# Kernel tuning notes

Measured on AMD Instinct MI355X. Metric: run time of the kernel, lower is better.

## Reference

```python
import jax, jax.numpy as jnp
import numpy as np
import math

D = 1024
H = 16
HEAD_D = D // H  # 64
T = 2048
B = 4


def setup_inputs() -> dict:
    key = jax.random.key(0)
    k1, k2, k3 = jax.random.split(key, 3)
    x = jax.random.normal(k1, (B, T, D), dtype=jnp.float32)
    # c_attn: Linear(d, d + 2*head_d, bias=False) -> weight applied as x @ W
    w_attn = jax.random.normal(k2, (D, D + 2 * HEAD_D), dtype=jnp.float32) * (1.0 / math.sqrt(D))
    w_proj = jax.random.normal(k3, (D, D), dtype=jnp.float32) * (1.0 / math.sqrt(D))
    return {"x": x, "w_attn": w_attn, "w_proj": w_proj}


def reference(x, w_attn, w_proj):
    Bv, Tv, _ = x.shape
    qkv = x @ w_attn  # [B,T,D+2*head_d]
    q = qkv[..., :D].reshape(Bv, Tv, H, HEAD_D).transpose(0, 2, 1, 3)  # [B,H,T,hd]
    k = qkv[..., D:D + HEAD_D]        # [B,T,hd] single shared KV head
    v = qkv[..., D + HEAD_D:]         # [B,T,hd]
    scale = 1.0 / math.sqrt(HEAD_D)
    # att: [B,H,T,T], shared K broadcast over H query heads
    att = jnp.einsum('bhqd,bkd->bhqk', q, k) * scale
    causal = jnp.tril(jnp.ones((Tv, Tv), dtype=bool))  # [T,T]
    att = jnp.where(causal[None, None, :, :], att, -jnp.inf)
    att = jax.nn.softmax(att, axis=-1)
    y = jnp.einsum('bhqk,bkd->bhqd', att, v)           # [B,H,T,hd]
    y = y.transpose(0, 2, 1, 3).reshape(Bv, Tv, D)     # [B,T,D]
    return y @ w_proj
```

## Files before the change

kernel.cpp:

```cpp
#include <hip/hip_runtime.h>

typedef unsigned short u16;
typedef unsigned int u32;
typedef __attribute__((ext_vector_type(8))) short short8;
typedef __attribute__((ext_vector_type(4))) float f32x4;
typedef __attribute__((ext_vector_type(4))) u16 u16x4;

__device__ __forceinline__ u16 f2bf(float f) {
  union { float f; unsigned u; } x; x.f = f;
  unsigned r = (x.u + 0x7fffu + ((x.u >> 16) & 1u)) >> 16;
  return (u16)r;
}

__device__ __forceinline__ u16 f2bf_rna(float f) {
  union { float f; u32 u; } x; x.f = f;
  return (u16)((x.u + 0x8000u) >> 16);
}

__device__ __forceinline__ f32x4 mfma16(short8 a, short8 b, f32x4 c) {
  return __builtin_amdgcn_mfma_f32_16x16x32_bf16(a, b, c, 0, 0, 0);
}

__device__ __forceinline__ void gload16(const u16* g, u16* l) {
  __builtin_amdgcn_global_load_lds((const __attribute__((address_space(1))) void*)g,
                                   (__attribute__((address_space(3))) void*)l, 16, 0, 0);
}

__global__ __launch_bounds__(256) void prep(const float* __restrict__ x,
                                            const float* __restrict__ w_attn,
                                            const float* __restrict__ w_proj,
                                            u16* __restrict__ xb,
                                            u16* __restrict__ wat,
                                            u16* __restrict__ wpt) {
  __shared__ float tile[32][33];
  const int bid = blockIdx.x, tid = threadIdx.x;
  if (bid >= 2176) {
    const int id = bid - 2176;
    const f32x4* src = (const f32x4*)(x + (size_t)id * 4096);
    u16x4* dst = (u16x4*)(xb + (size_t)id * 4096);
#pragma unroll
    for (int c = 0; c < 4; ++c) {
      f32x4 v = src[c * 256 + tid];
      u16x4 o;
#pragma unroll
      for (int j = 0; j < 4; ++j) o[j] = f2bf(v[j]);
      dst[c * 256 + tid] = o;
    }
    return;
  }
  const float* src; u16* dst; int C, bx, by;
  if (bid < 1152) { src = w_attn; dst = wat; C = 1152; bx = bid % 36; by = bid / 36; }
  else { int id = bid - 1152; src = w_proj; dst = wpt; C = 1024; bx = id & 31; by = id >> 5; }
  const int R = 1024;
  const int tx = tid & 31, ty = tid >> 5;
  int c = bx * 32 + tx, r0 = by * 32;
#pragma unroll
  for (int i = 0; i < 32; i += 8)
    tile[ty + i][tx] = src[(size_t)(r0 + ty + i) * C + c];
  __syncthreads();
  int oc = r0 + tx, orow0 = bx * 32;
#pragma unroll
  for (int i = 0; i < 32; i += 8)
    dst[(size_t)(orow0 + ty + i) * R + oc] = f2bf(tile[tx][ty + i]);
}

template <bool C_F32, bool VT>
__global__ __launch_bounds__(256) void gemm_bt(const u16* __restrict__ A,
                                               const u16* __restrict__ Bt,
                                               void* __restrict__ Cp,
                                               u16* __restrict__ vt,
                                               int lda, int ldb, int ldc, int K) {
  __shared__ u16 As[2][128 * 32];
  __shared__ u16 Bs[2][128 * 32];
  const int tid = threadIdx.x;
  const int wid = tid >> 6, lane = tid & 63;
  const int quad = lane >> 4, l15 = lane & 15;
  const int m0 = blockIdx.x * 128, n0 = blockIdx.y * 128;
  const int wm = (wid & 1) * 64, wn = (wid >> 1) * 64;
  const int sr = tid >> 2;
  const int sc = (tid & 3) * 8;

  f32x4 acc[4][4] = {};

  auto stage = [&](int t, int bb) {
    const int k0 = t << 5;
#pragma unroll
    for (int cch = 0; cch < 2; ++cch) {
      const int row = sr + cch * 64;
      gload16(A + (size_t)(m0 + row) * lda + k0 + sc, &As[bb][wid * 512 + cch * 2048]);
      gload16(Bt + (size_t)(n0 + row) * ldb + k0 + sc, &Bs[bb][wid * 512 + cch * 2048]);
    }
  };

  const int nk = K >> 5;
  stage(0, 0);
  for (int t = 0; t < nk; ++t) {
    const int bb = t & 1;
    __syncthreads();
    if (t + 1 < nk) stage(t + 1, bb ^ 1);
    short8 a[4], b[4];
#pragma unroll
    for (int i = 0; i < 4; ++i) a[i] = *(const short8*)&As[bb][(wm + 16 * i + l15) * 32 + quad * 8];
#pragma unroll
    for (int j = 0; j < 4; ++j) b[j] = *(const short8*)&Bs[bb][(wn + 16 * j + l15) * 32 + quad * 8];
#pragma unroll
    for (int i = 0; i < 4; ++i)
#pragma unroll
      for (int j = 0; j < 4; ++j)
        acc[i][j] = mfma16(a[i], b[j], acc[i][j]);
  }

#pragma unroll
  for (int i = 0; i < 4; ++i) {
#pragma unroll
    for (int j = 0; j < 4; ++j) {
      const int mrow = m0 + wm + 16 * i + quad * 4;
      const int ncol = n0 + wn + 16 * j + l15;
#pragma unroll
      for (int r = 0; r < 4; ++r) {
        float v = acc[i][j][r];
        if (C_F32) {
          ((float*)Cp)[(size_t)(mrow + r) * ldc + ncol] = v;
        } else {
          u16 hv = f2bf(v);
          ((u16*)Cp)[(size_t)(mrow + r) * ldc + ncol] = hv;
          if (VT) {
            if (ncol >= 1088) {
              int mg = mrow + r;
              int bb2 = mg >> 11, tt = mg & 2047;
              vt[(size_t)(bb2 * 64 + (ncol - 1088)) * 2048 + tt] = hv;
            }
          }
        }
      }
    }
  }
}

__global__ __launch_bounds__(256) void attn_kernel(const u16* __restrict__ qkv,
                                                   const u16* __restrict__ vt,
                                                   u16* __restrict__ y) {
  const int T = 2048, LD = 1152;
  __shared__ u16 Ks[64 * 68];
  __shared__ u16 Vts[64 * 68];
  __shared__ u16 Pw[4][2][16 * 68];

  const int bid = blockIdx.x;
  const int qt = 15 - (bid >> 6);
  const int bh = bid & 63, b = bh >> 4, h = bh & 15;
  const int q0 = qt * 128;
  const int tid = threadIdx.x, wid = tid >> 6, lane = tid & 63;
  const int quad = lane >> 4, l15 = lane & 15;
  const int wq = wid * 32;
  const u16* qkvb = qkv + (size_t)b * T * LD;
  const u16* vtb = vt + (size_t)b * 64 * 2048;
  const int sr0 = tid >> 3, sc0 = (tid & 7) * 8;
  const int sr1 = sr0 + 32;
  const float c1 = 0.18033688f;
  const float M = 18.0f;
  short8 ones;
#pragma unroll
  for (int j = 0; j < 8; ++j) ones[j] = (short)0x3F80;

  short8 qreg[2][2];
#pragma unroll
  for (int jt = 0; jt < 2; ++jt)
#pragma unroll
    for (int ks = 0; ks < 2; ++ks)
      qreg[jt][ks] = *(const short8*)(qkvb + (size_t)(q0 + wq + 16 * jt + l15) * LD + h * 64 + ks * 32 + quad * 8);

  f32x4 acc[4][2] = {};
  f32x4 accs[2] = {};

  short8 kr0 = *(const short8*)(qkvb + (size_t)sr0 * LD + 1024 + sc0);
  short8 kr1 = *(const short8*)(qkvb + (size_t)sr1 * LD + 1024 + sc0);
  short8 vr0 = *(const short8*)(vtb + (size_t)sr0 * 2048 + sc0);
  short8 vr1 = *(const short8*)(vtb + (size_t)sr1 * 2048 + sc0);

  const int ktmax = 2 * qt + 2;
  for (int kt = 0; kt < ktmax; ++kt) {
    const int kv0 = kt * 64;
    __syncthreads();
    *(short8*)&Ks[sr0 * 68 + sc0] = kr0;
    *(short8*)&Ks[sr1 * 68 + sc0] = kr1;
    *(short8*)&Vts[sr0 * 68 + sc0] = vr0;
    *(short8*)&Vts[sr1 * 68 + sc0] = vr1;
    __syncthreads();
    if (kt + 1 < ktmax) {
      const int nv0 = kv0 + 64;
      kr0 = *(const short8*)(qkvb + (size_t)(nv0 + sr0) * LD + 1024 + sc0);
      kr1 = *(const short8*)(qkvb + (size_t)(nv0 + sr1) * LD + 1024 + sc0);
      vr0 = *(const short8*)(vtb + (size_t)sr0 * 2048 + nv0 + sc0);
      vr1 = *(const short8*)(vtb + (size_t)sr1 * 2048 + nv0 + sc0);
    }
    if (kv0 > q0 + wq + 31) continue;

    f32x4 st[4][2] = {};
#pragma unroll
    for (int ks = 0; ks < 2; ++ks) {
      short8 kf[4];
#pragma unroll
      for (int i = 0; i < 4; ++i) kf[i] = *(const short8*)&Ks[(16 * i + l15) * 68 + ks * 32 + quad * 8];
#pragma unroll
      for (int i = 0; i < 4; ++i)
#pragma unroll
        for (int jt = 0; jt < 2; ++jt)
          st[i][jt] = mfma16(kf[i], qreg[jt][ks], st[i][jt]);
    }

    const bool needMask = (kv0 + 63 > q0 + wq);
#pragma unroll
    for (int jt = 0; jt < 2; ++jt) {
      u16* pw = &Pw[wid][jt][0];
      const int qg = q0 + wq + 16 * jt + l15;
#pragma unroll
      for (int i = 0; i < 4; ++i) {
        u16x4 pk;
#pragma unroll
        for (int r = 0; r < 4; ++r) {
          float p = __builtin_amdgcn_exp2f(fmaf(st[i][jt][r], c1, -M));
          if (needMask && (kv0 + 16 * i + quad * 4 + r > qg)) p = 0.f;
          pk[r] = f2bf_rna(p);
        }
        *(u16x4*)&pw[l15 * 68 + 16 * i + quad * 4] = pk;
      }
    }

#pragma unroll
    for (int ks = 0; ks < 2; ++ks) {
      short8 pf[2];
#pragma unroll
      for (int jt = 0; jt < 2; ++jt)
        pf[jt] = *(const short8*)&Pw[wid][jt][l15 * 68 + ks * 32 + quad * 8];
#pragma unroll
      for (int id = 0; id < 4; ++id) {
        short8 vf = *(const short8*)&Vts[(16 * id + l15) * 68 + ks * 32 + quad * 8];
        acc[id][0] = mfma16(vf, pf[0], acc[id][0]);
        acc[id][1] = mfma16(vf, pf[1], acc[id][1]);
      }
      accs[0] = mfma16(ones, pf[0], accs[0]);
      accs[1] = mfma16(ones, pf[1], accs[1]);
    }
  }

#pragma unroll
  for (int jt = 0; jt < 2; ++jt) {
    const float inv = 1.f / accs[jt][0];
    const int qg = q0 + wq + 16 * jt + l15;
#pragma unroll
    for (int id = 0; id < 4; ++id) {
      u16x4 o;
#pragma unroll
      for (int r = 0; r < 4; ++r) o[r] = f2bf(acc[id][jt][r] * inv);
      *(u16x4*)(y + (size_t)(b * T + qg) * 1024 + h * 64 + 16 * id + quad * 4) = o;
    }
  }
}

extern "C" void kernel_launch(void* const* d_in, const int* in_sizes, int n_in,
                              void* d_out, int out_size, void* d_ws, size_t ws_size,
                              hipStream_t stream) {
  const float* x = (const float*)d_in[0];
  const float* w_attn = (const float*)d_in[1];
  const float* w_proj = (const float*)d_in[2];
  float* out = (float*)d_out;
  char* ws = (char*)d_ws;

  u16* wat = (u16*)ws;
  u16* wpt = (u16*)(ws + 2359296);
  u16* xb  = (u16*)(ws + 4456448);
  u16* qkv = (u16*)(ws + 21233664);
  u16* vt  = (u16*)(ws + 40108032);
  u16* y   = (u16*)(ws + 41156608);

  prep<<<dim3(4224), dim3(256), 0, stream>>>(x, w_attn, w_proj, xb, wat, wpt);
  gemm_bt<false, true><<<dim3(64, 9), 256, 0, stream>>>(xb, wat, qkv, vt, 1024, 1024, 1152, 1024);
  attn_kernel<<<dim3(1024), dim3(256), 0, stream>>>(qkv, vt, y);
  gemm_bt<true, false><<<dim3(64, 8), 256, 0, stream>>>(y, wpt, out, nullptr, 1024, 1024, 1024, 1024);
}
```

Baseline: 209.4 us.

## Halve P scratch LDS, use packed bf16 convert, target five blocks per SM

The per-wave P staging buffer shrinks from two 16-row tiles to one, reused sequentially for the two query sub-tiles, which cuts shared memory per block. Float-to-bf16 conversion now uses the hardware v_cvt_pk_bf16_f32 instruction instead of manual integer rounding. Launch bounds request a minimum of five blocks per CU. Together these aim to raise occupancy and trim ALU work in the softmax stage, at the cost of extra LDS round trips and register pressure limits that could cause spills.

```diff
diff --git a/kernel.cpp b/kernel.cpp
--- a/kernel.cpp
+++ b/kernel.cpp
@@ -5,16 +5,12 @@
 typedef __attribute__((ext_vector_type(8))) short short8;
 typedef __attribute__((ext_vector_type(4))) float f32x4;
 typedef __attribute__((ext_vector_type(4))) u16 u16x4;
+typedef __attribute__((ext_vector_type(2))) u32 u32x2;
 
 __device__ __forceinline__ u16 f2bf(float f) {
   union { float f; unsigned u; } x; x.f = f;
   unsigned r = (x.u + 0x7fffu + ((x.u >> 16) & 1u)) >> 16;
   return (u16)r;
-}
-
-__device__ __forceinline__ u16 f2bf_rna(float f) {
-  union { float f; u32 u; } x; x.f = f;
-  return (u16)((x.u + 0x8000u) >> 16);
 }
 
 __device__ __forceinline__ f32x4 mfma16(short8 a, short8 b, f32x4 c) {
@@ -137,13 +133,13 @@
   }
 }
 
-__global__ __launch_bounds__(256) void attn_kernel(const u16* __restrict__ qkv,
-                                                   const u16* __restrict__ vt,
-                                                   u16* __restrict__ y) {
+__global__ __launch_bounds__(256, 5) void attn_kernel(const u16* __restrict__ qkv,
+                                                      const u16* __restrict__ vt,
+                                                      u16* __restrict__ y) {
   const int T = 2048, LD = 1152;
   __shared__ u16 Ks[64 * 68];
   __shared__ u16 Vts[64 * 68];
-  __shared__ u16 Pw[4][2][16 * 68];
+  __shared__ u16 Pw[4][16 * 68];
 
   const int bid = blockIdx.x;
   const int qt = 15 - (bid >> 6);
@@ -176,6 +172,8 @@
   short8 kr1 = *(const short8*)(qkvb + (size_t)sr1 * LD + 1024 + sc0);
   short8 vr0 = *(const short8*)(vtb + (size_t)sr0 * 2048 + sc0);
   short8 vr1 = *(const short8*)(vtb + (size_t)sr1 * 2048 + sc0);
+
+  u16* pw = &Pw[wid][0];
 
   const int ktmax = 2 * qt + 2;
   for (int kt = 0; kt < ktmax; ++kt) {
@@ -209,37 +207,64 @@
     }
 
     const bool needMask = (kv0 + 63 > q0 + wq);
-#pragma unroll
-    for (int jt = 0; jt < 2; ++jt) {
-      u16* pw = &Pw[wid][jt][0];
-      const int qg = q0 + wq + 16 * jt + l15;
+
+    u32 pk0[4][2], pk1[4][2];
+    {
+      const int qg = q0 + wq + l15;
 #pragma unroll
       for (int i = 0; i < 4; ++i) {
-        u16x4 pk;
+        float p[4];
 #pragma unroll
         for (int r = 0; r < 4; ++r) {
-          float p = __builtin_amdgcn_exp2f(fmaf(st[i][jt][r], c1, -M));
-          if (needMask && (kv0 + 16 * i + quad * 4 + r > qg)) p = 0.f;
-          pk[r] = f2bf_rna(p);
+          p[r] = __builtin_amdgcn_exp2f(fmaf(st[i][0][r], c1, -M));
+          if (needMask && (kv0 + 16 * i + quad * 4 + r > qg)) p[r] = 0.f;
         }
-        *(u16x4*)&pw[l15 * 68 + 16 * i + quad * 4] = pk;
+        asm("v_cvt_pk_bf16_f32 %0, %1, %2" : "=v"(pk0[i][0]) : "v"(p[0]), "v"(p[1]));
+        asm("v_cvt_pk_bf16_f32 %0, %1, %2" : "=v"(pk0[i][1]) : "v"(p[2]), "v"(p[3]));
       }
     }
+#pragma unroll
+    for (int i = 0; i < 4; ++i) {
+      u32x2 t; t[0] = pk0[i][0]; t[1] = pk0[i][1];
+      *(u32x2*)&pw[l15 * 68 + 16 * i + 4 * quad] = t;
+    }
+    {
+      const int qg = q0 + wq + 16 + l15;
+#pragma unroll
+      for (int i = 0; i < 4; ++i) {
+        float p[4];
+#pragma unroll
+        for (int r = 0; r < 4; ++r) {
+          p[r] = __builtin_amdgcn_exp2f(fmaf(st[i][1][r], c1, -M));
+          if (needMask && (kv0 + 16 * i + quad * 4 + r > qg)) p[r] = 0.f;
+        }
+        asm("v_cvt_pk_bf16_f32 %0, %1, %2" : "=v"(pk1[i][0]) : "v"(p[0]), "v"(p[1]));
+        asm("v_cvt_pk_bf16_f32 %0, %1, %2" : "=v"(pk1[i][1]) : "v"(p[2]), "v"(p[3]));
+      }
+    }
+    short8 pf[2][2];
+#pragma unroll
+    for (int ks = 0; ks < 2; ++ks)
+      pf[0][ks] = *(const short8*)&pw[l15 * 68 + ks * 32 + quad * 8];
+#pragma unroll
+    for (int i = 0; i < 4; ++i) {
+      u32x2 t; t[0] = pk1[i][0]; t[1] = pk1[i][1];
+      *(u32x2*)&pw[l15 * 68 + 16 * i + 4 * quad] = t;
+    }
+#pragma unroll
+    for (int ks = 0; ks < 2; ++ks)
+      pf[1][ks] = *(const short8*)&pw[l15 * 68 + ks * 32 + quad * 8];
 
 #pragma unroll
     for (int ks = 0; ks < 2; ++ks) {
-      short8 pf[2];
-#pragma unroll
-      for (int jt = 0; jt < 2; ++jt)
-        pf[jt] = *(const short8*)&Pw[wid][jt][l15 * 68 + ks * 32 + quad * 8];
 #pragma unroll
       for (int id = 0; id < 4; ++id) {
         short8 vf = *(const short8*)&Vts[(16 * id + l15) * 68 + ks * 32 + quad * 8];
-        acc[id][0] = mfma16(vf, pf[0], acc[id][0]);
-        acc[id][1] = mfma16(vf, pf[1], acc[id][1]);
+        acc[id][0] = mfma16(vf, pf[0][ks], acc[id][0]);
+        acc[id][1] = mfma16(vf, pf[1][ks], acc[id][1]);
       }
-      accs[0] = mfma16(ones, pf[0], accs[0]);
-      accs[1] = mfma16(ones, pf[1], accs[1]);
+      accs[0] = mfma16(ones, pf[0][ks], accs[0]);
+      accs[1] = mfma16(ones, pf[1][ks], accs[1]);
     }
   }
 
```

New measurement: 332.1 us. 1.59x slower.
